# Optimization experiments

Measured on AMD Instinct MI355X. Metric: run time of the kernel, lower is better.

Reference implementation:

```python
import jax, jax.numpy as jnp
import numpy as np
from jax import lax

N = 100000   # input points
M = 100000   # output points
CIN = 64
COUT = 64
K = 3        # cubic kernel size
G = 50       # grid side (points live at voxel centers of a G^3 grid)
SHIFT = 1    # coordinate shift so border queries (coord -1) stay non-negative
B = 64       # per-axis encode base, > G + K; key fits easily in int32


def _encode(c):
    # c: [..., 3] int32 xyz voxel coords -> unique int32 key
    c = c + SHIFT
    return (c[..., 2] * B + c[..., 1]) * B + c[..., 0]


def setup_inputs() -> dict:
    rng = np.random.RandomState(0)
    total = G ** 3

    def decode(idx):
        x = idx % G
        y = (idx // G) % G
        z = idx // (G * G)
        # +0.5 moves points to voxel centers (as in the layer's docstring example)
        return np.stack([x, y, z], axis=1).astype(np.float32) + 0.5

    inp_positions = jnp.asarray(decode(rng.permutation(total)[:N]))
    out_positions = jnp.asarray(decode(rng.permutation(total)[:M]))

    key = jax.random.key(0)
    k1, k2 = jax.random.split(key, 2)
    inp_features = jax.random.normal(k1, (N, CIN), jnp.float32)
    kernel = jax.random.normal(k2, (K, K, K, CIN, COUT), jnp.float32) * 0.05
    bias = jnp.zeros((COUT,), jnp.float32)
    voxel_size = jnp.ones((), jnp.float32)
    return {
        "inp_features": inp_features,
        "inp_positions": inp_positions,
        "out_positions": out_positions,
        "voxel_size": voxel_size,
        "kernel": kernel,
        "bias": bias,
    }


def reference(inp_features, inp_positions, out_positions, voxel_size, kernel, bias):
    # SparseConv on a regular grid: odd cubic kernel -> offset = 0, Linf radius
    # K*voxel*0.51 selects exactly the K^3 voxel neighborhood. Nearest-neighbor
    # interpolation with identity mapping maps relative offset d in [-r, r]^3
    # to filter tap index d + r on each axis (x = width = last spatial dim).
    inp_coord = jnp.floor(inp_positions / voxel_size).astype(jnp.int32)  # [N,3]
    out_coord = jnp.floor(out_positions / voxel_size).astype(jnp.int32)  # [M,3]

    # sorted-key hash table over input voxels
    keys = _encode(inp_coord)                    # [N]
    order = jnp.argsort(keys)
    skeys = keys[order]
    feats = inp_features[order]                  # [N, Cin]

    r = K // 2
    K3 = K ** 3
    ks = jnp.arange(K3)
    # flat kernel order is (z, y, x) to match kernel.reshape(K3, Cin, Cout)
    d_xyz = jnp.stack([ks % K - r, (ks // K) % K - r, ks // (K * K) - r],
                      axis=1).astype(jnp.int32)  # [K3, 3]
    Kmat = kernel.reshape(K3, CIN, COUT)

    n_inp = skeys.shape[0]

    def step(acc, xs):
        d, W = xs                                 # d: [3], W: [Cin, Cout]
        qk = _encode(out_coord + d)               # [M]
        p = jnp.searchsorted(skeys, qk)
        pc = jnp.clip(p, 0, n_inp - 1)
        found = (skeys[pc] == qk)[:, None]        # [M, 1]
        g = jnp.where(found, feats[pc], 0.0)      # [M, Cin]
        return acc + g @ W, None

    out0 = jnp.zeros((out_coord.shape[0], COUT), inp_features.dtype)
    out, _ = lax.scan(step, out0, (d_xyz, Kmat))
    return out + bias
```

## Files before the change

### kernel.cpp

```cpp
#include <hip/hip_runtime.h>
#include <math.h>

#define GY 54
#define ZD 58
#define NROWS (ZD*GY*64)

#define HX 10
#define HY 6
#define HXY 60
#define NH 600
#define NBX 7
#define NBY 13
#define NBZ 7
#define NBRICK (NBX*NBY*NBZ)
#define SLAB 80

#define K3CC (27*64*64)

typedef __bf16  bf16x8 __attribute__((ext_vector_type(8)));
typedef float  f32x16 __attribute__((ext_vector_type(16)));

#define AS1 __attribute__((address_space(1)))
#define AS3 __attribute__((address_space(3)))
#define GLD_LDS16(g, l) \
    __builtin_amdgcn_global_load_lds((const AS1 void*)(g), (AS3 void*)(l), 16, 0, 0)

__global__ void prep_kernel(const float* __restrict__ ipos, int n,
                            const float* __restrict__ opos, int m,
                            const float* __restrict__ vsp,
                            const float* __restrict__ W,
                            const float* __restrict__ feats,
                            int* __restrict__ imap, int* __restrict__ ikey,
                            int* __restrict__ omap, int* __restrict__ okey,
                            __bf16* __restrict__ Wt4,
                            __bf16* __restrict__ zrow,
                            __bf16* __restrict__ featsB) {
    int i = blockIdx.x * 256 + threadIdx.x;
    float vs = vsp[0];
    if (i < n) {
        int x = (int)floorf(ipos[3*i+0] / vs) + 1;
        int y = (int)floorf(ipos[3*i+1] / vs) + 1;
        int z = (int)floorf(ipos[3*i+2] / vs) + 1;
        int key = (z * GY + y) * 64 + x;
        ikey[i] = key;
        imap[key] = i;
    } else if (i < n + m) {
        int j = i - n;
        int x = (int)floorf(opos[3*j+0] / vs) + 1;
        int y = (int)floorf(opos[3*j+1] / vs) + 1;
        int z = (int)floorf(opos[3*j+2] / vs) + 1;
        int key = (z * GY + y) * 64 + x;
        okey[j] = key;
        omap[key] = j;
    } else if (i < n + m + K3CC) {
        int k  = i - n - m;
        int t  = k >> 12;
        int r  = k & 4095;
        int ci = r >> 6;
        int co = r & 63;
        int p   = ci >> 4;
        int cil = ci & 15;
        Wt4[(((p * 27 + t) << 6) + co) * 16 + cil] = (__bf16)W[k];
    } else if (i < n + m + K3CC + 32) {
        zrow[i - n - m - K3CC] = (__bf16)0.f;
    } else {
        int j = i - n - m - K3CC - 32;
        if (j < n * 8) {
            const float4* s = (const float4*)(feats + (size_t)j * 8);
            float4 f0 = s[0], f1 = s[1];
            bf16x8 v;
            v[0]=(__bf16)f0.x; v[1]=(__bf16)f0.y; v[2]=(__bf16)f0.z; v[3]=(__bf16)f0.w;
            v[4]=(__bf16)f1.x; v[5]=(__bf16)f1.y; v[6]=(__bf16)f1.z; v[7]=(__bf16)f1.w;
            *(bf16x8*)(featsB + (size_t)j * 8) = v;
        }
    }
}

__global__ __launch_bounds__(256, 2) void conv_kernel(
    const __bf16* __restrict__ featsB,
    const __bf16* __restrict__ Wt4,
    const __bf16* __restrict__ zrow,
    const float* __restrict__ bias,
    const int*   __restrict__ imap,
    const int*   __restrict__ ikey,
    const int*   __restrict__ omap,
    const int*   __restrict__ okey,
    float*       __restrict__ out,
    int N, int M)
{
    __shared__ __align__(16) __bf16 halo[2 * NH * 16];
    __shared__ int ridx[NH];
    __shared__ int obuf[256];

    const int tid = threadIdx.x;

    int q = (blockIdx.x & 7) * SLAB + (blockIdx.x >> 3);
    if (q >= NBRICK) return;
    const int bx = q % NBX;
    int rem = q / NBX;
    const int by = rem % NBY;
    const int bz = rem / NBY;

    #pragma unroll
    for (int it = 0; it < 3; ++it) {
        int r = it * 256 + tid;
        if (r < NH) {
            int xs = r % HX;
            int t2 = r / HX;
            int ys = t2 % HY;
            int zs = t2 / HY;
            int key = ((bz*8 + zs) * GY + (by*4 + ys)) * 64 + (bx*8 + xs);
            int idx = imap[key];
            int c = min(max(idx, 0), N - 1);
            ridx[r] = (idx >= 0 && idx < N && ikey[c] == key) ? idx : -1;
        }
    }
    {
        int x = tid & 7, y = (tid >> 3) & 3, z = tid >> 5;
        int key = ((bz*8 + z + 1) * GY + (by*4 + y + 1)) * 64 + (bx*8 + x + 1);
        int o = omap[key];
        int c = min(max(o, 0), M - 1);
        obuf[tid] = (o >= 0 && o < M && okey[c] == key) ? o : -1;
    }

    const int wave  = tid >> 6;
    const int lane  = tid & 63;
    const int lrow  = lane & 31;
    const int halfk = lane >> 5;
    const int xv = lrow & 7, yv = (lrow >> 3) & 3;
    const int arow0 = (2*wave + 1) * HXY + (yv + 1) * HX + (xv + 1);

    f32x16 acc00, acc01, acc10, acc11;
    #pragma unroll
    for (int i = 0; i < 16; ++i) { acc00[i]=0.f; acc01[i]=0.f; acc10[i]=0.f; acc11[i]=0.f; }

    __syncthreads();

    #pragma unroll
    for (int it = 0; it < 5; ++it) {
        int task = it * 256 + tid;
        if (task < NH * 2) {
            int r  = task >> 1;
            int hl = task & 1;
            int idx = ridx[r];
            const __bf16* src = (idx >= 0) ? featsB + (size_t)idx * 64 + hl * 8
                                           : zrow;
            GLD_LDS16(src, (char*)halo + task * 16);
        }
    }
    __syncthreads();

    #pragma unroll 1
    for (int p = 0; p < 4; ++p) {
        const __bf16* Ab0 = halo + (p & 1) * (NH * 16) + arow0 * 16 + halfk * 8;
        const __bf16* Bg0 = Wt4 + (size_t)p * 27648 + lrow * 16 + halfk * 8;

        bf16x8 rb0[4], rb1[4];
        #pragma unroll
        for (int i = 0; i < 4; ++i) {
            rb0[i] = *(const bf16x8*)(Bg0 + i * 1024);
            rb1[i] = *(const bf16x8*)(Bg0 + i * 1024 + 512);
        }

        if (p < 3) {
            char* dst = (char*)halo + ((p + 1) & 1) * (NH * 16 * 2);
            #pragma unroll
            for (int it = 0; it < 5; ++it) {
                int task = it * 256 + tid;
                if (task < NH * 2) {
                    int r  = task >> 1;
                    int hl = task & 1;
                    int idx = ridx[r];
                    const __bf16* src = (idx >= 0)
                        ? featsB + (size_t)idx * 64 + (p + 1) * 16 + hl * 8
                        : zrow;
                    GLD_LDS16(src, dst + task * 16);
                }
            }
        }

        #pragma unroll
        for (int t = 0; t < 27; ++t) {
            const int drow = (t/9 - 1)*HXY + ((t/3)%3 - 1)*HX + (t%3 - 1);
            bf16x8 a0 = *(const bf16x8*)(Ab0 + drow * 16);
            bf16x8 a1 = *(const bf16x8*)(Ab0 + (drow + HXY) * 16);
            bf16x8 b0 = rb0[t & 3];
            bf16x8 b1 = rb1[t & 3];
            if (t + 4 < 27) {
                rb0[t & 3] = *(const bf16x8*)(Bg0 + (t + 4) * 1024);
                rb1[t & 3] = *(const bf16x8*)(Bg0 + (t + 4) * 1024 + 512);
            }
            acc00 = __builtin_amdgcn_mfma_f32_32x32x16_bf16(a0, b0, acc00, 0, 0, 0);
            acc01 = __builtin_amdgcn_mfma_f32_32x32x16_bf16(a0, b1, acc01, 0, 0, 0);
            acc10 = __builtin_amdgcn_mfma_f32_32x32x16_bf16(a1, b0, acc10, 0, 0, 0);
            acc11 = __builtin_amdgcn_mfma_f32_32x32x16_bf16(a1, b1, acc11, 0, 0, 0);
        }

        if (p < 3) __syncthreads();
    }

    const int col0 = lrow, col1 = 32 + lrow;
    const float bv0 = bias[col0], bv1 = bias[col1];
    #pragma unroll
    for (int r = 0; r < 16; ++r) {
        int mrow = (r & 3) + 8 * (r >> 2) + 4 * halfk;
        int o0 = obuf[(2*wave)     * 32 + mrow];
        int o1 = obuf[(2*wave + 1) * 32 + mrow];
        if (o0 >= 0) {
            out[(size_t)o0 * 64 + col0] = acc00[r] + bv0;
            out[(size_t)o0 * 64 + col1] = acc01[r] + bv1;
        }
        if (o1 >= 0) {
            out[(size_t)o1 * 64 + col0] = acc10[r] + bv0;
            out[(size_t)o1 * 64 + col1] = acc11[r] + bv1;
        }
    }
}

extern "C" void kernel_launch(void* const* d_in, const int* in_sizes, int n_in,
                              void* d_out, int out_size, void* d_ws, size_t ws_size,
                              hipStream_t stream) {
    const float* feats = (const float*)d_in[0];
    const float* ipos  = (const float*)d_in[1];
    const float* opos  = (const float*)d_in[2];
    const float* vsp   = (const float*)d_in[3];
    const float* W     = (const float*)d_in[4];
    const float* bias  = (const float*)d_in[5];

    int N = in_sizes[0] / 64;
    int M = out_size / 64;

    int*    imap   = (int*)d_ws;
    int*    omap   = imap + NROWS;
    int*    ikey   = omap + NROWS;
    int*    okey   = ikey + N;
    __bf16* Wt4    = (__bf16*)(okey + M);
    __bf16* zrow   = Wt4 + K3CC;
    __bf16* featsB = zrow + 32;

    int total = N + M + K3CC + 32 + N * 8;
    prep_kernel<<<(total + 255) / 256, 256, 0, stream>>>(ipos, N, opos, M, vsp, W, feats,
                                                         imap, ikey, omap, okey,
                                                         Wt4, zrow, featsB);
    conv_kernel<<<8 * SLAB, 256, 0, stream>>>(featsB, Wt4, zrow, bias,
                                              imap, ikey, omap, okey,
                                              (float*)d_out, N, M);
}
```

Measured before the change: 136.0 us.

## Halve brick depth to 128-thread blocks and drop weight register prefetch

Each brick shrinks from 8x4x8 to 8x4x4 output voxels, with 128 threads per block and a 360-row halo. This roughly doubles the block count from about 637 to about 1183, which should fill the CUs better. The cost is a higher halo-to-interior ratio, so more redundant gathers per output. The 4-deep register ring that prefetched weights is replaced by direct per-tap loads, which frees registers but may expose global load latency in the MFMA loop.

```diff
diff --git a/kernel.cpp b/kernel.cpp
--- a/kernel.cpp
+++ b/kernel.cpp
@@ -8,12 +8,12 @@
 #define HX 10
 #define HY 6
 #define HXY 60
-#define NH 600
+#define NH2 360
 #define NBX 7
 #define NBY 13
-#define NBZ 7
-#define NBRICK (NBX*NBY*NBZ)
-#define SLAB 80
+#define NBZ2 13
+#define NBLK (NBX*NBY*NBZ2)
+#define SLABH 148
 
 #define K3CC (27*64*64)
 
@@ -76,7 +76,7 @@
     }
 }
 
-__global__ __launch_bounds__(256, 2) void conv_kernel(
+__global__ __launch_bounds__(128, 2) void conv_kernel(
     const __bf16* __restrict__ featsB,
     const __bf16* __restrict__ Wt4,
     const __bf16* __restrict__ zrow,
@@ -88,36 +88,36 @@
     float*       __restrict__ out,
     int N, int M)
 {
-    __shared__ __align__(16) __bf16 halo[2 * NH * 16];
-    __shared__ int ridx[NH];
-    __shared__ int obuf[256];
+    __shared__ __align__(16) __bf16 halo[2 * NH2 * 16];
+    __shared__ int ridx[NH2];
+    __shared__ int obuf[128];
 
     const int tid = threadIdx.x;
 
-    int q = (blockIdx.x & 7) * SLAB + (blockIdx.x >> 3);
-    if (q >= NBRICK) return;
+    int q = (blockIdx.x & 7) * SLABH + (blockIdx.x >> 3);
+    if (q >= NBLK) return;
     const int bx = q % NBX;
     int rem = q / NBX;
-    const int by = rem % NBY;
-    const int bz = rem / NBY;
+    const int by  = rem % NBY;
+    const int bz2 = rem / NBY;
 
     #pragma unroll
     for (int it = 0; it < 3; ++it) {
-        int r = it * 256 + tid;
-        if (r < NH) {
+        int r = it * 128 + tid;
+        if (r < NH2) {
             int xs = r % HX;
             int t2 = r / HX;
             int ys = t2 % HY;
             int zs = t2 / HY;
-            int key = ((bz*8 + zs) * GY + (by*4 + ys)) * 64 + (bx*8 + xs);
+            int key = ((bz2*4 + zs) * GY + (by*4 + ys)) * 64 + (bx*8 + xs);
             int idx = imap[key];
             int c = min(max(idx, 0), N - 1);
             ridx[r] = (idx >= 0 && idx < N && ikey[c] == key) ? idx : -1;
         }
     }
     {
-        int x = tid & 7, y = (tid >> 3) & 3, z = tid >> 5;
-        int key = ((bz*8 + z + 1) * GY + (by*4 + y + 1)) * 64 + (bx*8 + x + 1);
+        int x = tid & 7, y = (tid >> 3) & 3, z2 = tid >> 5;
+        int key = ((bz2*4 + z2 + 1) * GY + (by*4 + y + 1)) * 64 + (bx*8 + x + 1);
         int o = omap[key];
         int c = min(max(o, 0), M - 1);
         obuf[tid] = (o >= 0 && o < M && okey[c] == key) ? o : -1;
@@ -137,9 +137,9 @@
     __syncthreads();
 
     #pragma unroll
-    for (int it = 0; it < 5; ++it) {
-        int task = it * 256 + tid;
-        if (task < NH * 2) {
+    for (int it = 0; it < 6; ++it) {
+        int task = it * 128 + tid;
+        if (task < NH2 * 2) {
             int r  = task >> 1;
             int hl = task & 1;
             int idx = ridx[r];
@@ -152,22 +152,15 @@
 
     #pragma unroll 1
     for (int p = 0; p < 4; ++p) {
-        const __bf16* Ab0 = halo + (p & 1) * (NH * 16) + arow0 * 16 + halfk * 8;
+        const __bf16* Ab0 = halo + (p & 1) * (NH2 * 16) + arow0 * 16 + halfk * 8;
         const __bf16* Bg0 = Wt4 + (size_t)p * 27648 + lrow * 16 + halfk * 8;
 
-        bf16x8 rb0[4], rb1[4];
-        #pragma unroll
-        for (int i = 0; i < 4; ++i) {
-            rb0[i] = *(const bf16x8*)(Bg0 + i * 1024);
-            rb1[i] = *(const bf16x8*)(Bg0 + i * 1024 + 512);
-        }
-
         if (p < 3) {
-            char* dst = (char*)halo + ((p + 1) & 1) * (NH * 16 * 2);
+            char* dst = (char*)halo + ((p + 1) & 1) * (NH2 * 16 * 2);
             #pragma unroll
-            for (int it = 0; it < 5; ++it) {
-                int task = it * 256 + tid;
-                if (task < NH * 2) {
+            for (int it = 0; it < 6; ++it) {
+                int task = it * 128 + tid;
+                if (task < NH2 * 2) {
                     int r  = task >> 1;
                     int hl = task & 1;
                     int idx = ridx[r];
@@ -184,12 +177,8 @@
             const int drow = (t/9 - 1)*HXY + ((t/3)%3 - 1)*HX + (t%3 - 1);
             bf16x8 a0 = *(const bf16x8*)(Ab0 + drow * 16);
             bf16x8 a1 = *(const bf16x8*)(Ab0 + (drow + HXY) * 16);
-            bf16x8 b0 = rb0[t & 3];
-            bf16x8 b1 = rb1[t & 3];
-            if (t + 4 < 27) {
-                rb0[t & 3] = *(const bf16x8*)(Bg0 + (t + 4) * 1024);
-                rb1[t & 3] = *(const bf16x8*)(Bg0 + (t + 4) * 1024 + 512);
-            }
+            bf16x8 b0 = *(const bf16x8*)(Bg0 + t * 1024);
+            bf16x8 b1 = *(const bf16x8*)(Bg0 + t * 1024 + 512);
             acc00 = __builtin_amdgcn_mfma_f32_32x32x16_bf16(a0, b0, acc00, 0, 0, 0);
             acc01 = __builtin_amdgcn_mfma_f32_32x32x16_bf16(a0, b1, acc01, 0, 0, 0);
             acc10 = __builtin_amdgcn_mfma_f32_32x32x16_bf16(a1, b0, acc10, 0, 0, 0);
@@ -242,7 +231,7 @@
     prep_kernel<<<(total + 255) / 256, 256, 0, stream>>>(ipos, N, opos, M, vsp, W, feats,
                                                          imap, ikey, omap, okey,
                                                          Wt4, zrow, featsB);
-    conv_kernel<<<8 * SLAB, 256, 0, stream>>>(featsB, Wt4, zrow, bias,
-                                              imap, ikey, omap, okey,
-                                              (float*)d_out, N, M);
+    conv_kernel<<<8 * SLABH, 128, 0, stream>>>(featsB, Wt4, zrow, bias,
+                                               imap, ikey, omap, okey,
+                                               (float*)d_out, N, M);
 }
```

Measured after the change: 132.3 us (median of 2 runs). -2.7%, faster.
